# Kernel tuning notes

Measured on AMD Instinct MI355X. Metric: run time of the kernel, lower is better.

## Reference

```python
import jax, jax.numpy as jnp
import numpy as np


def setup_inputs() -> dict:
    key = jax.random.key(0)
    k1, k2 = jax.random.split(key)
    queries = jax.random.normal(k1, (16, 1024, 256), dtype=jnp.float32)
    embedding = jax.random.normal(k2, (8192, 256), dtype=jnp.float32) * 0.02
    return {"queries": queries, "embedding": embedding}


def reference(queries, embedding):
    commitment_weight = 0.25
    # squared L2 distances: ||q||^2 + ||e||^2 - 2 q.e  -> [b, k, n]
    q_sq = jnp.sum(queries * queries, axis=-1, keepdims=True)          # [b,k,1]
    e_sq = jnp.sum(embedding * embedding, axis=-1)[None, None, :]      # [1,1,n]
    distances = q_sq + e_sq - 2.0 * jnp.einsum('bkc,nc->bkn', queries, embedding)
    code_indices = jnp.argmin(distances, axis=-1)                      # [b,k] int
    quantized = embedding[code_indices]                                # [b,k,c]
    commit_loss = jnp.mean((jax.lax.stop_gradient(queries) - quantized) ** 2)
    codebook_loss = jnp.mean((queries - jax.lax.stop_gradient(quantized)) ** 2)
    vq_loss = codebook_loss + commitment_weight * commit_loss
    # straight-through estimator
    quantized_st = queries + jax.lax.stop_gradient(quantized - queries)
    return (code_indices, quantized_st, vq_loss)
```

## Files before the change

kernel.cpp:

```cpp
#include <hip/hip_runtime.h>
#include <float.h>

typedef _Float16 half8 __attribute__((ext_vector_type(8)));
typedef _Float16 half4v __attribute__((ext_vector_type(4)));
typedef float f32x4 __attribute__((ext_vector_type(4)));

#define M_TOTAL 16384
#define N_CODES 8192
#define KDIM    256
#define BM 128
#define BN 256
#define BK 32
#define NK (KDIM / BK)
#define NB (N_CODES / BN)
#define TS 32
#define MARGIN 3.6e-3f
#define SQ_SCALE 512.0f
#define SE_SCALE 2048.0f
#define INV_PROD 1.9073486328125e-06f
#define RG 4
#define RCODES 1024
#define RNCH (N_CODES / RCODES)
#define RPB 1024
#define RM_BLOCKS 256
#define LR_BLOCKS 32

__global__ void prep_kernel(const float* __restrict__ src, _Float16* __restrict__ dst,
                            float* __restrict__ sq, float scale) {
    const int tid = threadIdx.x;
    const int row0 = blockIdx.x * 4;
    {
        const int r = row0 + (tid >> 6);
        const int e4 = tid & 63;
        const float4 v = *(const float4*)(src + (size_t)r * KDIM + e4 * 4);
        const half4v h = {(_Float16)(v.x * scale), (_Float16)(v.y * scale),
                          (_Float16)(v.z * scale), (_Float16)(v.w * scale)};
        ((half4v*)(dst + (size_t)r * KDIM))[e4] = h;
    }
    if (tid < 64) {
        const int grp = tid >> 4;
        const int sub = tid & 15;
        const int row = row0 + grp;
        const float* p = src + (size_t)row * KDIM + (sub >> 3) * 128 + (sub & 7);
        float r;
        {
            #pragma clang fp contract(off)
            float v = p[0];
            r = v * v;
            #pragma unroll
            for (int k = 1; k < 16; k++) { const float w = p[k * 8]; r = r + w * w; }
        }
        const float t1 = r  + __shfl_xor(r,  1, 64);
        const float t2 = t1 + __shfl_xor(t1, 2, 64);
        const float t3 = t2 + __shfl_xor(t2, 4, 64);
        const float t4 = t3 + __shfl_xor(t3, 8, 64);
        if (sub == 0) sq[row] = t4;
    }
}

__global__ void transpose_kernel(const float* __restrict__ E, float* __restrict__ ET) {
    __shared__ float tile[64][65];
    const int n0 = blockIdx.x * 64;
    const int k0 = blockIdx.y * 64;
    const int tid = threadIdx.x;
    const int r = tid >> 4;
    const int c4 = tid & 15;
    #pragma unroll
    for (int p = 0; p < 4; p++) {
        const int row = p * 16 + r;
        const float4 v = *(const float4*)(E + (size_t)(n0 + row) * KDIM + k0 + c4 * 4);
        tile[row][c4 * 4 + 0] = v.x;
        tile[row][c4 * 4 + 1] = v.y;
        tile[row][c4 * 4 + 2] = v.z;
        tile[row][c4 * 4 + 3] = v.w;
    }
    __syncthreads();
    #pragma unroll
    for (int p = 0; p < 4; p++) {
        const int d = p * 16 + r;
        float4 o;
        o.x = tile[c4 * 4 + 0][d];
        o.y = tile[c4 * 4 + 1][d];
        o.z = tile[c4 * 4 + 2][d];
        o.w = tile[c4 * 4 + 3][d];
        *(float4*)(ET + (size_t)(k0 + d) * N_CODES + n0 + c4 * 4) = o;
    }
}

union SMemU {
    struct { _Float16 q[2][BM * TS]; _Float16 e[2][BN * TS]; } t;
    struct { unsigned k1[BM][2]; unsigned k2[BM][2]; } red;
};

__device__ __forceinline__ void gl_lds16(const void* g, void* lds) {
    __builtin_amdgcn_global_load_lds(
        (const __attribute__((address_space(1))) unsigned*)g,
        (__attribute__((address_space(3))) unsigned*)lds, 16, 0, 0);
}

__global__ __launch_bounds__(256, 2)
void mfma_top2_kernel(const _Float16* __restrict__ Qh, const _Float16* __restrict__ Eh,
                      const float* __restrict__ esq,
                      unsigned* __restrict__ k1s, unsigned* __restrict__ k2s) {
    __shared__ SMemU sm;
    const int tid = threadIdx.x;
    const int m0 = blockIdx.x * BM;
    const int n0 = blockIdx.y * BN;
    const int w = tid >> 6, lane = tid & 63;
    const int wm = w >> 1, wn = w & 1;
    const int qd = lane >> 4, c = lane & 15;

    const int lrow = lane >> 2;
    const int gsw = (lane & 3) ^ ((lane >> 3) & 3);
    const _Float16* qsrc = Qh + (size_t)(m0 + w * 32 + lrow) * KDIM + gsw * 8;
    const _Float16* esrc = Eh + (size_t)(n0 + w * 64 + lrow) * KDIM + gsw * 8;

    f32x4 acc[4][8];
    const f32x4 zero = {0.f, 0.f, 0.f, 0.f};
    #pragma unroll
    for (int mt = 0; mt < 4; mt++)
        #pragma unroll
        for (int nt = 0; nt < 8; nt++) acc[mt][nt] = zero;

    #define STAGE(buf, kofs) do {                                                  \
        _Float16* qdst = sm.t.q[buf] + w * 1024;                                   \
        _Float16* edst = sm.t.e[buf] + w * 2048;                                   \
        gl_lds16(qsrc + (kofs),             qdst);                                 \
        gl_lds16(qsrc + 16 * KDIM + (kofs), qdst + 512);                           \
        gl_lds16(esrc + (kofs),             edst);                                 \
        gl_lds16(esrc + 16 * KDIM + (kofs), edst + 512);                           \
        gl_lds16(esrc + 32 * KDIM + (kofs), edst + 1024);                          \
        gl_lds16(esrc + 48 * KDIM + (kofs), edst + 1536);                          \
    } while (0)

    STAGE(0, 0);
    __syncthreads();

    const int csw = (c >> 1) & 3;

    for (int ki = 0; ki < NK; ki++) {
        if (ki + 1 < NK) STAGE((ki + 1) & 1, (ki + 1) * BK);
        const _Float16* bq = sm.t.q[ki & 1];
        const _Float16* be = sm.t.e[ki & 1];
        half8 qa[4];
        #pragma unroll
        for (int mt = 0; mt < 4; mt++)
            qa[mt] = *(const half8*)(bq + (wm * 64 + mt * 16 + c) * TS + (qd ^ csw) * 8);
        #pragma unroll
        for (int nt = 0; nt < 8; nt++) {
            const half8 eh = *(const half8*)(be + (wn * 128 + nt * 16 + c) * TS + (qd ^ csw) * 8);
            #pragma unroll
            for (int mt = 0; mt < 4; mt++)
                acc[mt][nt] = __builtin_amdgcn_mfma_f32_16x16x32_f16(qa[mt], eh, acc[mt][nt], 0, 0, 0);
        }
        __syncthreads();
    }
    #undef STAGE

    float es8[8];
    #pragma unroll
    for (int nt = 0; nt < 8; nt++) es8[nt] = esq[n0 + wn * 128 + nt * 16 + c] + 8.0f;

    unsigned k1[16], k2[16];
    #pragma unroll
    for (int i = 0; i < 16; i++) { k1[i] = 0xFFFFFFFFu; k2[i] = 0xFFFFFFFFu; }

    #pragma unroll
    for (int mt = 0; mt < 4; mt++)
        #pragma unroll
        for (int nt = 0; nt < 8; nt++) {
            const unsigned nl = (unsigned)(wn * 128 + nt * 16 + c);
            #pragma unroll
            for (int r = 0; r < 4; r++) {
                const int i = mt * 4 + r;
                const float d = fmaf(acc[mt][nt][r], -INV_PROD, es8[nt]);
                const unsigned k = (__float_as_uint(d) & 0xFFFFFF00u) | nl;
                const unsigned t = min(k1[i], k);
                k2[i] = min(k2[i], max(k1[i], k));
                k1[i] = t;
            }
        }
    #pragma unroll
    for (int s = 1; s < 16; s <<= 1) {
        #pragma unroll
        for (int i = 0; i < 16; i++) {
            const unsigned ok1 = (unsigned)__shfl_xor((int)k1[i], s, 64);
            const unsigned ok2 = (unsigned)__shfl_xor((int)k2[i], s, 64);
            const unsigned t = min(k1[i], ok1);
            k2[i] = min(min(k2[i], ok2), max(k1[i], ok1));
            k1[i] = t;
        }
    }
    __syncthreads();
    if (c == 0) {
        #pragma unroll
        for (int mt = 0; mt < 4; mt++)
            #pragma unroll
            for (int r = 0; r < 4; r++) {
                const int ml = wm * 64 + mt * 16 + qd * 4 + r;
                sm.red.k1[ml][wn] = k1[mt * 4 + r];
                sm.red.k2[ml][wn] = k2[mt * 4 + r];
            }
    }
    __syncthreads();
    if (tid < BM) {
        const unsigned a1 = sm.red.k1[tid][0], b1 = sm.red.k1[tid][1];
        const unsigned a2 = sm.red.k2[tid][0], b2 = sm.red.k2[tid][1];
        const size_t o = (size_t)(m0 + tid) * NB + blockIdx.y;
        k1s[o] = min(a1, b1);
        k2s[o] = min(min(a2, b2), max(a1, b1));
    }
}

__global__ void finalize_kernel(const float* __restrict__ Q, const float* __restrict__ E,
                                const unsigned* __restrict__ k1s, const unsigned* __restrict__ k2s,
                                int* __restrict__ fcount, int* __restrict__ flist,
                                float* __restrict__ ws_loss, float* __restrict__ out) {
    const int q = blockIdx.x * 4 + (threadIdx.x >> 6);
    const int lane = threadIdx.x & 63;
    unsigned d1 = 0xFFFFFF00u;
    unsigned d2 = 0xFFFFFF00u;
    int gi = 0x7FFFFFFF;
    if (lane < NB) {
        const unsigned k1 = k1s[(size_t)q * NB + lane];
        const unsigned k2 = k2s[(size_t)q * NB + lane];
        d1 = k1 & 0xFFFFFF00u;
        gi = lane * BN + (int)(k1 & 255u);
        d2 = k2 & 0xFFFFFF00u;
    }
    #pragma unroll
    for (int s = 1; s < 64; s <<= 1) {
        const unsigned od1 = (unsigned)__shfl_xor((int)d1, s, 64);
        const int      ogi = __shfl_xor(gi, s, 64);
        const unsigned od2 = (unsigned)__shfl_xor((int)d2, s, 64);
        const unsigned nd2 = min(min(d2, od2), max(d1, od1));
        const bool take = (od1 < d1) || (od1 == d1 && ogi < gi);
        d1 = take ? od1 : d1;
        gi = take ? ogi : gi;
        d2 = nd2;
    }
    if ((__uint_as_float(d2) - __uint_as_float(d1)) < MARGIN) {
        if (lane == 0) flist[atomicAdd(fcount, 1)] = q;
        return;
    }

    if (lane == 0) out[q] = (float)gi;
    const float4 qv = *(const float4*)(Q + (size_t)q * KDIM + lane * 4);
    const float4 ev = *(const float4*)(E + (size_t)gi * KDIM + lane * 4);
    float4 st;
    {
        #pragma clang fp contract(off)
        st.x = qv.x + (ev.x - qv.x);
        st.y = qv.y + (ev.y - qv.y);
        st.z = qv.z + (ev.z - qv.z);
        st.w = qv.w + (ev.w - qv.w);
    }
    *(float4*)(out + M_TOTAL + (size_t)q * KDIM + lane * 4) = st;

    const float dx = qv.x - ev.x, dy = qv.y - ev.y, dz = qv.z - ev.z, dw = qv.w - ev.w;
    float s = dx * dx + dy * dy + dz * dz + dw * dw;
    #pragma unroll
    for (int off = 32; off > 0; off >>= 1) s += __shfl_down(s, off);
    if (lane == 0) ws_loss[q] = s;
}

__global__ __launch_bounds__(256, 4)
void refine_partial_kernel(const float* __restrict__ Q, const float* __restrict__ ET,
                           const float* __restrict__ qsq, const float* __restrict__ esq,
                           const int* __restrict__ fcount, const int* __restrict__ flist,
                           float* __restrict__ rp_v, int* __restrict__ rp_i) {
    const int cnt = *fcount;
    if (cnt == 0) return;
    const int ngroups = (cnt + RG - 1) / RG;
    const int ntasks = ngroups * RNCH;
    const int tid = threadIdx.x;
    const int w = tid >> 6, lane = tid & 63;
    __shared__ float qs[RG][KDIM];
    __shared__ float redv[4][RG];
    __shared__ int   redi[4][RG];

    for (int t = blockIdx.x; t < ntasks; t += RPB) {
        const int grp = t >> 3;
        const int chunk = t & (RNCH - 1);
        __syncthreads();
        {
            const int g = tid >> 6, c4 = tid & 63;
            const int fi = min(grp * RG + g, cnt - 1);
            const int q = flist[fi];
            *(float4*)&qs[g][c4 * 4] = *(const float4*)(Q + (size_t)q * KDIM + c4 * 4);
        }
        __syncthreads();

        const int nb = chunk * RCODES + tid * 4;
        float a[RG][4];
        #pragma unroll
        for (int g = 0; g < RG; g++)
            #pragma unroll
            for (int j = 0; j < 4; j++) a[g][j] = 0.f;

        for (int k4 = 0; k4 < KDIM / 4; k4++) {
            float4 qv[RG];
            #pragma unroll
            for (int g = 0; g < RG; g++) qv[g] = *(const float4*)&qs[g][k4 * 4];
            #pragma unroll
            for (int kk = 0; kk < 4; kk++) {
                const float4 ev = *(const float4*)(ET + (size_t)(k4 * 4 + kk) * N_CODES + nb);
                #pragma unroll
                for (int g = 0; g < RG; g++) {
                    const float qk = (kk == 0) ? qv[g].x : (kk == 1) ? qv[g].y
                                   : (kk == 2) ? qv[g].z : qv[g].w;
                    a[g][0] = fmaf(qk, ev.x, a[g][0]);
                    a[g][1] = fmaf(qk, ev.y, a[g][1]);
                    a[g][2] = fmaf(qk, ev.z, a[g][2]);
                    a[g][3] = fmaf(qk, ev.w, a[g][3]);
                }
            }
        }

        float es[4];
        #pragma unroll
        for (int j = 0; j < 4; j++) es[j] = esq[nb + j];

        #pragma unroll
        for (int g = 0; g < RG; g++) {
            const int fi = min(grp * RG + g, cnt - 1);
            const float qsv = qsq[flist[fi]];
            float bv = FLT_MAX; int bi = 0x7fffffff;
            #pragma unroll
            for (int j = 0; j < 4; j++) {
                float d;
                {
                    #pragma clang fp contract(off)
                    const float t1 = qsv + es[j];
                    d = t1 - 2.0f * a[g][j];
                }
                if (d < bv) { bv = d; bi = nb + j; }
            }
            #pragma unroll
            for (int s = 1; s < 64; s <<= 1) {
                const float ov = __shfl_xor(bv, s, 64);
                const int   oi = __shfl_xor(bi, s, 64);
                if (ov < bv || (ov == bv && oi < bi)) { bv = ov; bi = oi; }
            }
            if (lane == 0) { redv[w][g] = bv; redi[w][g] = bi; }
        }
        __syncthreads();
        if (tid < RG) {
            float fv = redv[0][tid]; int fidx = redi[0][tid];
            #pragma unroll
            for (int u = 1; u < 4; u++) {
                if (redv[u][tid] < fv || (redv[u][tid] == fv && redi[u][tid] < fidx)) {
                    fv = redv[u][tid]; fidx = redi[u][tid];
                }
            }
            rp_v[(size_t)t * RG + tid] = fv;
            rp_i[(size_t)t * RG + tid] = fidx;
        }
    }
}

__global__ void refine_merge_kernel(const float* __restrict__ Q, const float* __restrict__ E,
                                    const int* __restrict__ fcount, const int* __restrict__ flist,
                                    const float* __restrict__ rp_v, const int* __restrict__ rp_i,
                                    float* __restrict__ ws_loss, float* __restrict__ out) {
    const int cnt = *fcount;
    const int lane = threadIdx.x;
    for (int fi = blockIdx.x; fi < cnt; fi += RM_BLOCKS) {
        const int q = flist[fi];
        const int grp = fi >> 2, g = fi & 3;
        float bv = FLT_MAX; int bi = 0x7fffffff;
        if (lane < RNCH) {
            const size_t t = (size_t)(grp * RNCH + lane);
            bv = rp_v[t * RG + g];
            bi = rp_i[t * RG + g];
        }
        #pragma unroll
        for (int s = 1; s < 64; s <<= 1) {
            const float ov = __shfl_xor(bv, s, 64);
            const int   oi = __shfl_xor(bi, s, 64);
            if (ov < bv || (ov == bv && oi < bi)) { bv = ov; bi = oi; }
        }
        if (lane == 0) out[q] = (float)bi;

        const float4 qv = *(const float4*)(Q + (size_t)q * KDIM + lane * 4);
        const float4 ev = *(const float4*)(E + (size_t)bi * KDIM + lane * 4);
        float4 st;
        {
            #pragma clang fp contract(off)
            st.x = qv.x + (ev.x - qv.x);
            st.y = qv.y + (ev.y - qv.y);
            st.z = qv.z + (ev.z - qv.z);
            st.w = qv.w + (ev.w - qv.w);
        }
        *(float4*)(out + M_TOTAL + (size_t)q * KDIM + lane * 4) = st;
        const float dx = qv.x - ev.x, dy = qv.y - ev.y, dz = qv.z - ev.z, dw = qv.w - ev.w;
        float s = dx * dx + dy * dy + dz * dz + dw * dw;
        #pragma unroll
        for (int off = 32; off > 0; off >>= 1) s += __shfl_down(s, off);
        if (lane == 0) ws_loss[q] = s;
    }
}

__global__ void loss_reduce_kernel(const float* __restrict__ ws_loss, float* __restrict__ out) {
    const int tid = threadIdx.x;
    float s = 0.f;
    for (int i = blockIdx.x * 256 + tid; i < M_TOTAL; i += LR_BLOCKS * 256)
        s += ws_loss[i];
    #pragma unroll
    for (int off = 32; off > 0; off >>= 1) s += __shfl_down(s, off);
    __shared__ float ws[4];
    if ((tid & 63) == 0) ws[tid >> 6] = s;
    __syncthreads();
    if (tid == 0) {
        const float tot = (ws[0] + ws[1]) + (ws[2] + ws[3]);
        atomicAdd(out + M_TOTAL + (size_t)M_TOTAL * KDIM,
                  tot * (1.25f / (float)((size_t)M_TOTAL * KDIM)));
    }
}

extern "C" void kernel_launch(void* const* d_in, const int* in_sizes, int n_in,
                              void* d_out, int out_size, void* d_ws, size_t ws_size,
                              hipStream_t stream) {
    const float* Q = (const float*)d_in[0];
    const float* E = (const float*)d_in[1];
    float* out = (float*)d_out;

    char* ws = (char*)d_ws;
    _Float16* Qh  = (_Float16*)(ws);
    _Float16* Eh  = (_Float16*)(ws + (size_t)8  * 1024 * 1024);
    float* qsq    = (float*)   (ws + (size_t)12 * 1024 * 1024);
    float* esq    = qsq + M_TOTAL;
    unsigned* k1s = (unsigned*)(ws + (size_t)13 * 1024 * 1024);
    unsigned* k2s = (unsigned*)(ws + (size_t)17 * 1024 * 1024);
    int*   fcount = (int*)     (ws + (size_t)25 * 1024 * 1024);
    int*   flist  = fcount + 64;
    float* ws_loss= (float*)   (ws + (size_t)25 * 1024 * 1024 + 512 * 1024);
    float* ET     = (float*)   (ws + (size_t)26 * 1024 * 1024);
    float* rp_v   = (float*)k1s;
    int*   rp_i   = (int*)k2s;

    hipMemsetAsync(out + M_TOTAL + (size_t)M_TOTAL * KDIM, 0, sizeof(float), stream);
    hipMemsetAsync(fcount, 0, sizeof(int), stream);

    prep_kernel<<<M_TOTAL / 4, 256, 0, stream>>>(Q, Qh, qsq, SQ_SCALE);
    prep_kernel<<<N_CODES / 4, 256, 0, stream>>>(E, Eh, esq, SE_SCALE);
    transpose_kernel<<<dim3(N_CODES / 64, KDIM / 64), 256, 0, stream>>>(E, ET);

    mfma_top2_kernel<<<dim3(M_TOTAL / BM, N_CODES / BN), 256, 0, stream>>>(
        Qh, Eh, esq, k1s, k2s);

    finalize_kernel<<<M_TOTAL / 4, 256, 0, stream>>>(Q, E, k1s, k2s, fcount, flist, ws_loss, out);
    refine_partial_kernel<<<RPB, 256, 0, stream>>>(Q, ET, qsq, esq, fcount, flist, rp_v, rp_i);
    refine_merge_kernel<<<RM_BLOCKS, 64, 0, stream>>>(Q, E, fcount, flist, rp_v, rp_i, ws_loss, out);
    loss_reduce_kernel<<<LR_BLOCKS, 256, 0, stream>>>(ws_loss, out);
}
```

Measured before the change: 224.9 us.

## Triple-buffer MFMA K-loop with vmcnt waits and fuse prep/transpose launches

Fuses the three preprocessing launches (Q half conversion, E half conversion, E transpose) into one kernel that dispatches on block index, removing two launches. The main MFMA distance kernel moves from double to triple buffering of LDS tiles. It prefetches two stages ahead, uses explicit vmcnt waits with raw barriers instead of __syncthreads, raises wave priority around the MFMA block, and fully unrolls the K loop. The extra buffer increases LDS use, which may lower occupancy at two blocks per CU, and the hand-counted vmcnt values must match the number of loads issued per stage.

```diff
diff --git a/kernel.cpp b/kernel.cpp
--- a/kernel.cpp
+++ b/kernel.cpp
@@ -25,10 +25,14 @@
 #define RM_BLOCKS 256
 #define LR_BLOCKS 32
 
-__global__ void prep_kernel(const float* __restrict__ src, _Float16* __restrict__ dst,
-                            float* __restrict__ sq, float scale) {
-    const int tid = threadIdx.x;
-    const int row0 = blockIdx.x * 4;
+#define PREP_Q_BLOCKS (M_TOTAL / 4)
+#define PREP_E_BLOCKS (N_CODES / 4)
+#define TR_BLOCKS ((N_CODES / 64) * (KDIM / 64))
+
+__device__ __forceinline__ void prep_body(const float* __restrict__ src,
+                                          _Float16* __restrict__ dst,
+                                          float* __restrict__ sq, float scale,
+                                          int row0, int tid) {
     {
         const int r = row0 + (tid >> 6);
         const int e4 = tid & 63;
@@ -58,11 +62,24 @@
     }
 }
 
-__global__ void transpose_kernel(const float* __restrict__ E, float* __restrict__ ET) {
+__global__ void prep_fused_kernel(const float* __restrict__ Q, const float* __restrict__ E,
+                                  _Float16* __restrict__ Qh, _Float16* __restrict__ Eh,
+                                  float* __restrict__ qsq, float* __restrict__ esq,
+                                  float* __restrict__ ET) {
     __shared__ float tile[64][65];
-    const int n0 = blockIdx.x * 64;
-    const int k0 = blockIdx.y * 64;
     const int tid = threadIdx.x;
+    const int b = blockIdx.x;
+    if (b < PREP_Q_BLOCKS) {
+        prep_body(Q, Qh, qsq, SQ_SCALE, b * 4, tid);
+        return;
+    }
+    if (b < PREP_Q_BLOCKS + PREP_E_BLOCKS) {
+        prep_body(E, Eh, esq, SE_SCALE, (b - PREP_Q_BLOCKS) * 4, tid);
+        return;
+    }
+    const int idx = b - PREP_Q_BLOCKS - PREP_E_BLOCKS;
+    const int n0 = (idx & 127) * 64;
+    const int k0 = (idx >> 7) * 64;
     const int r = tid >> 4;
     const int c4 = tid & 15;
     #pragma unroll
@@ -88,7 +105,7 @@
 }
 
 union SMemU {
-    struct { _Float16 q[2][BM * TS]; _Float16 e[2][BN * TS]; } t;
+    struct { _Float16 q[3][BM * TS]; _Float16 e[3][BN * TS]; } t;
     struct { unsigned k1[BM][2]; unsigned k2[BM][2]; } red;
 };
 
@@ -134,18 +151,23 @@
     } while (0)
 
     STAGE(0, 0);
-    __syncthreads();
+    STAGE(1, BK);
+    STAGE(2, 2 * BK);
+    asm volatile("s_waitcnt vmcnt(12)" ::: "memory");
+    __builtin_amdgcn_s_barrier();
 
     const int csw = (c >> 1) & 3;
 
+    #pragma unroll
     for (int ki = 0; ki < NK; ki++) {
-        if (ki + 1 < NK) STAGE((ki + 1) & 1, (ki + 1) * BK);
-        const _Float16* bq = sm.t.q[ki & 1];
-        const _Float16* be = sm.t.e[ki & 1];
+        const int buf = ki % 3;
+        const _Float16* bq = sm.t.q[buf];
+        const _Float16* be = sm.t.e[buf];
         half8 qa[4];
         #pragma unroll
         for (int mt = 0; mt < 4; mt++)
             qa[mt] = *(const half8*)(bq + (wm * 64 + mt * 16 + c) * TS + (qd ^ csw) * 8);
+        __builtin_amdgcn_s_setprio(1);
         #pragma unroll
         for (int nt = 0; nt < 8; nt++) {
             const half8 eh = *(const half8*)(be + (wn * 128 + nt * 16 + c) * TS + (qd ^ csw) * 8);
@@ -153,7 +175,12 @@
             for (int mt = 0; mt < 4; mt++)
                 acc[mt][nt] = __builtin_amdgcn_mfma_f32_16x16x32_f16(qa[mt], eh, acc[mt][nt], 0, 0, 0);
         }
-        __syncthreads();
+        __builtin_amdgcn_s_setprio(0);
+        if (ki == NK - 1) break;
+        if (ki <= NK - 3) { asm volatile("s_waitcnt vmcnt(6)" ::: "memory"); }
+        else              { asm volatile("s_waitcnt vmcnt(0)" ::: "memory"); }
+        __builtin_amdgcn_s_barrier();
+        if (ki + 3 < NK) STAGE(buf, (ki + 3) * BK);
     }
     #undef STAGE
 
@@ -442,9 +469,8 @@
     hipMemsetAsync(out + M_TOTAL + (size_t)M_TOTAL * KDIM, 0, sizeof(float), stream);
     hipMemsetAsync(fcount, 0, sizeof(int), stream);
 
-    prep_kernel<<<M_TOTAL / 4, 256, 0, stream>>>(Q, Qh, qsq, SQ_SCALE);
-    prep_kernel<<<N_CODES / 4, 256, 0, stream>>>(E, Eh, esq, SE_SCALE);
-    transpose_kernel<<<dim3(N_CODES / 64, KDIM / 64), 256, 0, stream>>>(E, ET);
+    prep_fused_kernel<<<PREP_Q_BLOCKS + PREP_E_BLOCKS + TR_BLOCKS, 256, 0, stream>>>(
+        Q, E, Qh, Eh, qsq, esq, ET);
 
     mfma_top2_kernel<<<dim3(M_TOTAL / BM, N_CODES / BN), 256, 0, stream>>>(
         Qh, Eh, esq, k1s, k2s);
```

New measurement: 216.9 us. -3.5%, faster.
